# Optimization experiments

Hardware: AMD Instinct MI355X
Metric: run time of the kernel (lower is better)

## Reference

```python
import jax, jax.numpy as jnp
import numpy as np

D_MODEL = 1024
N_HEAD = 16
D_FF = 4096
SEG = 128  # hardcoded modality split length in the original module
EPS = 1e-5


def setup_inputs() -> dict:
    key = jax.random.key(0)
    ks = jax.random.split(key, 18)
    s = 0.02
    d, f = D_MODEL, D_FF
    inp = {
        "src": jax.random.normal(ks[0], (128, 256, d), dtype=jnp.float32),
        "Wq": jax.random.normal(ks[1], (d, d), dtype=jnp.float32) * s,
        "bq": jnp.zeros((d,), dtype=jnp.float32),
        "Wk": jax.random.normal(ks[2], (d, d), dtype=jnp.float32) * s,
        "bk": jnp.zeros((d,), dtype=jnp.float32),
        "Wv": jax.random.normal(ks[3], (d, d), dtype=jnp.float32) * s,
        "bv": jnp.zeros((d,), dtype=jnp.float32),
        "Wo": jax.random.normal(ks[4], (d, d), dtype=jnp.float32) * s,
        "bo": jnp.zeros((d,), dtype=jnp.float32),
        "W1": jax.random.normal(ks[5], (d, f), dtype=jnp.float32) * s,
        "b1": jnp.zeros((f,), dtype=jnp.float32),
        "W2": jax.random.normal(ks[6], (f, d), dtype=jnp.float32) * s,
        "b2": jnp.zeros((d,), dtype=jnp.float32),
        "g1": jnp.ones((SEG, d), dtype=jnp.float32),
        "beta1": jnp.zeros((SEG, d), dtype=jnp.float32),
        "g2": jnp.ones((SEG, d), dtype=jnp.float32),
        "beta2": jnp.zeros((SEG, d), dtype=jnp.float32),
    }
    return inp


def _mha(q_in, kv_in, Wq, bq, Wk, bk, Wv, bv, Wo, bo):
    B, Sq, d = q_in.shape
    Sk = kv_in.shape[1]
    dh = d // N_HEAD
    # project and split heads: [B, S, d] -> [B, H, S, dh]
    q = (q_in @ Wq + bq).reshape(B, Sq, N_HEAD, dh).transpose(0, 2, 1, 3)
    k = (kv_in @ Wk + bk).reshape(B, Sk, N_HEAD, dh).transpose(0, 2, 1, 3)
    v = (kv_in @ Wv + bv).reshape(B, Sk, N_HEAD, dh).transpose(0, 2, 1, 3)
    scores = jnp.einsum("bhqd,bhkd->bhqk", q, k) / jnp.sqrt(jnp.float32(dh))
    probs = jax.nn.softmax(scores, axis=-1)
    out = jnp.einsum("bhqk,bhkd->bhqd", probs, v)
    out = out.transpose(0, 2, 1, 3).reshape(B, Sq, d)
    return out @ Wo + bo


def _ln2d(x, g, b):
    # LayerNorm over last two dims (128, d_model), matching nn.LayerNorm((128, d))
    mu = jnp.mean(x, axis=(-2, -1), keepdims=True)
    var = jnp.mean(jnp.square(x - mu), axis=(-2, -1), keepdims=True)
    return (x - mu) * jax.lax.rsqrt(var + EPS) * g + b


def reference(src, Wq, bq, Wk, bk, Wv, bv, Wo, bo, W1, b1, W2, b2, g1, beta1, g2, beta2):
    modal1 = src[:, :SEG, :]
    modal2 = src[:, SEG:, :]

    def ffn(x):
        return jax.nn.relu(x @ W1 + b1) @ W2 + b2

    # modal1 attends to modal2
    m1 = modal1 + _mha(modal1, modal2, Wq, bq, Wk, bk, Wv, bv, Wo, bo)
    m1 = _ln2d(m1, g1, beta1)
    m1 = _ln2d(m1 + ffn(m1), g2, beta2)

    # modal2 attends to updated modal1
    m2 = modal2 + _mha(modal2, m1, Wq, bq, Wk, bk, Wv, bv, Wo, bo)
    m2 = _ln2d(m2, g1, beta1)
    m2 = _ln2d(m2 + ffn(m2), g2, beta2)

    return jnp.concatenate([m1, m2], axis=1)
```

## Files before the change

kernel.cpp:

```cpp
#include <hip/hip_runtime.h>
#include <stdint.h>

#define DEV __device__ __forceinline__

typedef __bf16 bf16x8 __attribute__((ext_vector_type(8)));
typedef float  f32x4  __attribute__((ext_vector_type(4)));

struct alignas(8) U16x4 { uint16_t x, y, z, w; };
struct alignas(16) U16x8 { uint16_t v[8]; };

DEV uint16_t f2bf(float f) {
  union { float f; uint32_t u; } v; v.f = f;
  uint32_t r = v.u + 0x7fffu + ((v.u >> 16) & 1u);
  return (uint16_t)(r >> 16);
}
DEV float bf2f(uint16_t u) {
  union { uint32_t u; float f; } v; v.u = ((uint32_t)u) << 16;
  return v.f;
}

DEV void gload16(const void* g, void* l) {
  __builtin_amdgcn_global_load_lds((__attribute__((address_space(1))) void*)(g),
                                   (__attribute__((address_space(3))) void*)(l),
                                   16, 0, 0);
}

__global__ __launch_bounds__(1024) void transpose_cvt(
    const float* __restrict__ in, uint16_t* __restrict__ out, int R, int C) {
  __shared__ float tile[32][33];
  const int tx = threadIdx.x, ty = threadIdx.y;
  const int r = blockIdx.y * 32 + ty, c = blockIdx.x * 32 + tx;
  tile[ty][tx] = in[(size_t)r * C + c];
  __syncthreads();
  const int oc = blockIdx.x * 32 + ty;
  const int orr = blockIdx.y * 32 + tx;
  out[(size_t)oc * R + orr] = f2bf(tile[tx][ty]);
}

__global__ __launch_bounds__(256) void cvt_modal(
    const float* __restrict__ src, uint16_t* __restrict__ m1, uint16_t* __restrict__ m2) {
  const int idx = blockIdx.x * 256 + threadIdx.x;
  const int E = idx * 4;
  const int t = E >> 10, dd = E & 1023;
  const size_t s1 = ((size_t)(t >> 7) * 256 + (t & 127)) * 1024 + dd;
  float4 a = *(const float4*)&src[s1];
  float4 b = *(const float4*)&src[s1 + 131072];
  U16x4 pa{f2bf(a.x), f2bf(a.y), f2bf(a.z), f2bf(a.w)};
  U16x4 pb{f2bf(b.x), f2bf(b.y), f2bf(b.z), f2bf(b.w)};
  *(U16x4*)&m1[E] = pa;
  *(U16x4*)&m2[E] = pb;
}

#define STA8(D, H, C, T) \
  gload16(Ac + (size_t)((H) * 2 + (C)) * kr64b + (size_t)(T) * 128 + aoff32, \
          &lds[(D) * 16384 + (H) * 8192 + (C) * 4096 + wS])
#define STB8(D, H, C, T) \
  gload16(Bc + (size_t)((H) * 2 + (C)) * kr64b + (size_t)(T) * 128 + boff32, \
          &lds[32768 + (D) * 16384 + (H) * 8192 + (C) * 4096 + wS])

#define PH8(Q, AB, BB, RDB, S1, S2, VMSTR)                                     \
  {                                                                            \
    if (RDB) {                                                                 \
      _Pragma("unroll") for (int n = 0; n < 4; ++n) {                          \
        bfr[n][0] = *(const bf16x8*)&lds[(BB) + bRow + n * 1024 + c0];         \
        bfr[n][1] = *(const bf16x8*)&lds[(BB) + bRow + n * 1024 + c1];         \
      }                                                                        \
    }                                                                          \
    _Pragma("unroll") for (int dm = 0; dm < 2; ++dm) {                         \
      afr[dm][0] = *(const bf16x8*)&lds[(AB) + aRow + ((Q) * 2 + dm) * 1024 + c0]; \
      afr[dm][1] = *(const bf16x8*)&lds[(AB) + aRow + ((Q) * 2 + dm) * 1024 + c1]; \
    }                                                                          \
    S1;                                                                        \
    S2;                                                                        \
    __builtin_amdgcn_s_barrier();                                              \
    asm volatile("s_waitcnt lgkmcnt(0)" ::: "memory");                         \
    __builtin_amdgcn_sched_barrier(0);                                         \
    __builtin_amdgcn_s_setprio(1);                                             \
    _Pragma("unroll") for (int dm = 0; dm < 2; ++dm)                           \
      _Pragma("unroll") for (int n = 0; n < 4; ++n) {                          \
        acc[(Q) * 2 + dm][n] = __builtin_amdgcn_mfma_f32_16x16x32_bf16(        \
            afr[dm][0], bfr[n][0], acc[(Q) * 2 + dm][n], 0, 0, 0);             \
        acc[(Q) * 2 + dm][n] = __builtin_amdgcn_mfma_f32_16x16x32_bf16(        \
            afr[dm][1], bfr[n][1], acc[(Q) * 2 + dm][n], 0, 0, 0);             \
      }                                                                        \
    __builtin_amdgcn_s_setprio(0);                                             \
    __builtin_amdgcn_sched_barrier(0);                                         \
    asm volatile(VMSTR ::: "memory");                                          \
    __builtin_amdgcn_s_barrier();                                              \
  }

#define ITER8(I, ST, VM4, VM8)                                                 \
  {                                                                            \
    const int t1 = 2 * (I) + 1, t2 = 2 * (I) + 2, t3 = 2 * (I) + 3;            \
    PH8(0, 0, 32768, 1, STA8(1, 0, 0, t1), STA8(1, 0, 1, t1), "")              \
    PH8(1, 0, 32768, 0, STA8(1, 1, 0, t1), STA8(1, 1, 1, t1), "")              \
    PH8(2, 0, 32768, 0, if (ST) STB8(0, 0, 0, t2), if (ST) STB8(0, 0, 1, t2), "") \
    PH8(3, 0, 32768, 0, if (ST) STB8(0, 1, 0, t2), if (ST) STB8(0, 1, 1, t2), VM4) \
    PH8(0, 16384, 49152, 1, if (ST) STA8(0, 0, 0, t2), if (ST) STA8(0, 0, 1, t2), "") \
    PH8(1, 16384, 49152, 0, if (ST) STA8(0, 1, 0, t2), if (ST) STA8(0, 1, 1, t2), "") \
    PH8(2, 16384, 49152, 0, if (ST) STB8(1, 0, 0, t3), if (ST) STB8(1, 0, 1, t3), "") \
    PH8(3, 16384, 49152, 0, if (ST) STB8(1, 1, 0, t3), if (ST) STB8(1, 1, 1, t3), VM8) \
  }

template <int RESID, bool RELU, bool OUTF32>
__global__ __launch_bounds__(512, 2) void gemm8p(
    const uint16_t* __restrict__ A, const uint16_t* __restrict__ Bt,
    const float* __restrict__ bias, const void* __restrict__ resid,
    void* __restrict__ outp, int N, int K, int nbn, int soff) {
  __shared__ __align__(16) uint16_t lds[65536];

  const int nwg = gridDim.x;
  const int s = (blockIdx.x & 7) * (nwg >> 3) + (blockIdx.x >> 3);
  const int bm = s / nbn, bn = s % nbn;
  const int brow = bm << 8, bcol = bn << 8;

  const int tid = threadIdx.x;
  const int w = tid >> 6, lane = tid & 63, l15 = lane & 15, lhi = lane >> 4;
  const int wm = w >> 2, wn = w & 3;

  const int cswz = (tid & 7) ^ ((tid >> 3) & 7);
  const uint32_t aoff32 =
      (uint32_t)(((size_t)(brow + (tid >> 3)) * (size_t)K + cswz * 8) * 2);
  const uint32_t boff32 =
      (uint32_t)(((size_t)(bcol + (tid >> 3)) * (size_t)K + cswz * 8) * 2);
  const char* Ac = (const char*)A;
  const char* Bc = (const char*)Bt;
  const uint32_t kr64b = (uint32_t)(64u * (uint32_t)K * 2u);
  const int wS = w * 512;

  const int c0 = (lhi ^ (l15 & 7)) * 8;
  const int c1 = c0 ^ 32;
  const int aRow = (wm * 128 + l15) * 64;
  const int bRow = (wn * 64 + l15) * 64;

  f32x4 acc[8][4];
  const f32x4 z = {0.f, 0.f, 0.f, 0.f};
#pragma unroll
  for (int m = 0; m < 8; ++m)
#pragma unroll
    for (int n = 0; n < 4; ++n) acc[m][n] = z;

  const int NI = K >> 7;

  STA8(0, 0, 0, 0); STA8(0, 0, 1, 0); STA8(0, 1, 0, 0); STA8(0, 1, 1, 0);
  STB8(0, 0, 0, 0); STB8(0, 0, 1, 0); STB8(0, 1, 0, 0); STB8(0, 1, 1, 0);
  STB8(1, 0, 0, 1); STB8(1, 0, 1, 1); STB8(1, 1, 0, 1); STB8(1, 1, 1, 1);
  asm volatile("s_waitcnt vmcnt(4)" ::: "memory");
  __builtin_amdgcn_s_barrier();
  __builtin_amdgcn_sched_barrier(0);

  {
    bf16x8 afr[2][2], bfr[4][2];
    int i = 0;
    for (; i < NI - 1; ++i)
      ITER8(i, true, "s_waitcnt vmcnt(4)", "s_waitcnt vmcnt(4)")
    ITER8(i, false, "s_waitcnt vmcnt(0)", "")
  }

#pragma unroll
  for (int n = 0; n < 4; ++n) {
    const int col = bcol + wn * 64 + n * 16 + l15;
    const float bs = bias[col];
#pragma unroll
    for (int m = 0; m < 8; ++m) {
#pragma unroll
      for (int r = 0; r < 4; ++r) {
        const int row = brow + wm * 128 + m * 16 + lhi * 4 + r;
        float v = acc[m][n][r] + bs;
        if (RELU) v = fmaxf(v, 0.f);
        if (RESID == 1) v += ((const float*)resid)[(size_t)row * 1024 + col];
        if (RESID == 2)
          v += ((const float*)resid)[((size_t)(row >> 7) * 256 + soff + (row & 127)) * 1024 + col];
        if (RESID == 3)
          v += bf2f(((const uint16_t*)resid)[(size_t)row * 1024 + col]);
        if (OUTF32)
          ((float*)outp)[(size_t)row * N + col] = v;
        else
          ((uint16_t*)outp)[(size_t)row * N + col] = f2bf(v);
      }
    }
  }
}

__global__ __launch_bounds__(256) void attn_kern(
    const uint16_t* __restrict__ Q, const uint16_t* __restrict__ KV,
    uint16_t* __restrict__ O) {
  __shared__ uint16_t sm[24576];
  uint16_t* sQ = sm;
  uint16_t* sK = sm + 8192;
  uint16_t* sVt = sm + 16384;
  uint16_t* sP = sm;
  const int bh = blockIdx.x, b = bh >> 4, h = bh & 15;
  const int tid = threadIdx.x, w = tid >> 6, lane = tid & 63, l15 = lane & 15, lhi = lane >> 4;
  const size_t base = (size_t)b * 131072 + h * 64;
  const size_t bkv = (size_t)b * 262144 + h * 64;

  for (int i = 0; i < 4; ++i) {
    const int gidx = i * 256 + tid;
    const int row = gidx >> 3, co = (gidx & 7) * 8;
    *(uint4*)&sQ[row * 64 + co] = *(const uint4*)&Q[base + (size_t)row * 1024 + co];
    *(uint4*)&sK[row * 64 + co] = *(const uint4*)&KV[bkv + (size_t)row * 2048 + co];
  }
  {
    const int r = tid >> 1, cb = (tid & 1) * 32;
    for (int jj = 0; jj < 4; ++jj) {
      uint4 vv = *(const uint4*)&KV[bkv + 1024 + (size_t)r * 2048 + cb + jj * 8];
      const uint16_t* e = (const uint16_t*)&vv;
      for (int j = 0; j < 8; ++j) sVt[(cb + jj * 8 + j) * 128 + r] = e[j];
    }
  }
  __syncthreads();

  f32x4 s[2][8];
  const f32x4 z = {0.f, 0.f, 0.f, 0.f};
  for (int m = 0; m < 2; ++m)
    for (int n = 0; n < 8; ++n) s[m][n] = z;
#pragma unroll
  for (int kk = 0; kk < 2; ++kk) {
    bf16x8 aq[2];
#pragma unroll
    for (int m = 0; m < 2; ++m)
      aq[m] = *(const bf16x8*)&sQ[(w * 32 + m * 16 + l15) * 64 + kk * 32 + lhi * 8];
#pragma unroll
    for (int n = 0; n < 8; ++n) {
      bf16x8 bk = *(const bf16x8*)&sK[(n * 16 + l15) * 64 + kk * 32 + lhi * 8];
#pragma unroll
      for (int m = 0; m < 2; ++m)
        s[m][n] = __builtin_amdgcn_mfma_f32_16x16x32_bf16(aq[m], bk, s[m][n], 0, 0, 0);
    }
  }

  for (int m = 0; m < 2; ++m) {
    float mx[4], sum[4];
#pragma unroll
    for (int r = 0; r < 4; ++r) {
      float v = s[m][0][r];
      for (int n = 1; n < 8; ++n) v = fmaxf(v, s[m][n][r]);
      for (int msk = 1; msk < 16; msk <<= 1) v = fmaxf(v, __shfl_xor(v, msk, 64));
      mx[r] = v;
      sum[r] = 0.f;
    }
    for (int n = 0; n < 8; ++n)
      for (int r = 0; r < 4; ++r) {
        float e = __expf((s[m][n][r] - mx[r]) * 0.125f);
        s[m][n][r] = e;
        sum[r] += e;
      }
#pragma unroll
    for (int r = 0; r < 4; ++r) {
      float t = sum[r];
      for (int msk = 1; msk < 16; msk <<= 1) t += __shfl_xor(t, msk, 64);
      sum[r] = 1.f / t;
    }
    for (int n = 0; n < 8; ++n)
      for (int r = 0; r < 4; ++r) s[m][n][r] *= sum[r];
  }
  __syncthreads();

  for (int m = 0; m < 2; ++m)
    for (int n = 0; n < 8; ++n)
      for (int r = 0; r < 4; ++r)
        sP[(w * 32 + m * 16 + lhi * 4 + r) * 128 + n * 16 + l15] = f2bf(s[m][n][r]);
  __syncthreads();

  f32x4 o[2][4];
  for (int m = 0; m < 2; ++m)
    for (int n = 0; n < 4; ++n) o[m][n] = z;
#pragma unroll
  for (int kk = 0; kk < 4; ++kk) {
    bf16x8 ap[2];
#pragma unroll
    for (int m = 0; m < 2; ++m)
      ap[m] = *(const bf16x8*)&sP[(w * 32 + m * 16 + l15) * 128 + kk * 32 + lhi * 8];
#pragma unroll
    for (int n = 0; n < 4; ++n) {
      bf16x8 bv = *(const bf16x8*)&sVt[(n * 16 + l15) * 128 + kk * 32 + lhi * 8];
#pragma unroll
      for (int m = 0; m < 2; ++m)
        o[m][n] = __builtin_amdgcn_mfma_f32_16x16x32_bf16(ap[m], bv, o[m][n], 0, 0, 0);
    }
  }
  for (int m = 0; m < 2; ++m)
    for (int n = 0; n < 4; ++n)
      for (int r = 0; r < 4; ++r) {
        const int q = w * 32 + m * 16 + lhi * 4 + r, c = n * 16 + l15;
        O[base + (size_t)q * 1024 + c] = f2bf(o[m][n][r]);
      }
}

__global__ __launch_bounds__(256) void ln_stats(
    const uint16_t* __restrict__ x, float* __restrict__ pstats) {
  const int b = blockIdx.x >> 2, q = blockIdx.x & 3, tid = threadIdx.x;
  const uint16_t* xb = x + (size_t)b * 131072 + q * 32768;
  float s = 0.f, ss = 0.f;
  for (int i = tid; i < 4096; i += 256) {
    U16x8 v = *(const U16x8*)&xb[i * 8];
#pragma unroll
    for (int j = 0; j < 8; ++j) {
      float f = bf2f(v.v[j]);
      s += f;
      ss += f * f;
    }
  }
#pragma unroll
  for (int m = 1; m < 64; m <<= 1) {
    s += __shfl_xor(s, m, 64);
    ss += __shfl_xor(ss, m, 64);
  }
  __shared__ float red[8];
  const int w = tid >> 6;
  if ((tid & 63) == 0) { red[w] = s; red[4 + w] = ss; }
  __syncthreads();
  if (tid == 0) {
    pstats[blockIdx.x * 2] = red[0] + red[1] + red[2] + red[3];
    pstats[blockIdx.x * 2 + 1] = red[4] + red[5] + red[6] + red[7];
  }
}

template <bool FINAL>
__global__ __launch_bounds__(256) void ln_apply(
    const uint16_t* __restrict__ x, const float* __restrict__ g,
    const float* __restrict__ bet, const float* __restrict__ pstats,
    uint16_t* __restrict__ outbf, float* __restrict__ outf) {
  const int b = blockIdx.x >> 4, c = blockIdx.x & 15, tid = threadIdx.x;
  float S = 0.f, SS = 0.f;
#pragma unroll
  for (int k = 0; k < 4; ++k) {
    S += pstats[b * 8 + k * 2];
    SS += pstats[b * 8 + k * 2 + 1];
  }
  const float mu = S * (1.f / 131072.f);
  const float rs = rsqrtf(SS * (1.f / 131072.f) - mu * mu + 1e-5f);
  const size_t xb = (size_t)b * 131072;
#pragma unroll
  for (int j = 0; j < 4; ++j) {
    const int o = c * 8192 + (j * 256 + tid) * 8;
    U16x8 v = *(const U16x8*)&x[xb + o];
    float4 g0 = *(const float4*)&g[o], g1 = *(const float4*)&g[o + 4];
    float4 b0 = *(const float4*)&bet[o], b1 = *(const float4*)&bet[o + 4];
    float r[8];
    r[0] = (bf2f(v.v[0]) - mu) * rs * g0.x + b0.x;
    r[1] = (bf2f(v.v[1]) - mu) * rs * g0.y + b0.y;
    r[2] = (bf2f(v.v[2]) - mu) * rs * g0.z + b0.z;
    r[3] = (bf2f(v.v[3]) - mu) * rs * g0.w + b0.w;
    r[4] = (bf2f(v.v[4]) - mu) * rs * g1.x + b1.x;
    r[5] = (bf2f(v.v[5]) - mu) * rs * g1.y + b1.y;
    r[6] = (bf2f(v.v[6]) - mu) * rs * g1.z + b1.z;
    r[7] = (bf2f(v.v[7]) - mu) * rs * g1.w + b1.w;
    if (FINAL) {
      float4 o0{r[0], r[1], r[2], r[3]}, o1{r[4], r[5], r[6], r[7]};
      float* of = outf + (size_t)b * 262144 + o;
      *(float4*)&of[0] = o0;
      *(float4*)&of[4] = o1;
      if (outbf) {
        U16x8 u;
#pragma unroll
        for (int i = 0; i < 8; ++i) u.v[i] = f2bf(r[i]);
        *(U16x8*)&outbf[xb + o] = u;
      }
    } else {
      U16x8 u;
#pragma unroll
      for (int i = 0; i < 8; ++i) u.v[i] = f2bf(r[i]);
      *(U16x8*)&outbf[xb + o] = u;
    }
  }
}

extern "C" void kernel_launch(void* const* d_in, const int* in_sizes, int n_in,
                              void* d_out, int out_size, void* d_ws, size_t ws_size,
                              hipStream_t stream) {
  const float* src = (const float*)d_in[0];
  const float* Wq = (const float*)d_in[1];
  const float* bq = (const float*)d_in[2];
  const float* Wk = (const float*)d_in[3];
  const float* bk = (const float*)d_in[4];
  const float* Wv = (const float*)d_in[5];
  const float* bv = (const float*)d_in[6];
  const float* Wo = (const float*)d_in[7];
  const float* bo = (const float*)d_in[8];
  const float* W1 = (const float*)d_in[9];
  const float* b1 = (const float*)d_in[10];
  const float* W2 = (const float*)d_in[11];
  const float* b2 = (const float*)d_in[12];
  const float* g1 = (const float*)d_in[13];
  const float* be1 = (const float*)d_in[14];
  const float* g2 = (const float*)d_in[15];
  const float* be2 = (const float*)d_in[16];
  float* dout = (float*)d_out;
  char* ws = (char*)d_ws;

  const size_t MB = 1024 * 1024;
  uint16_t* wq_t = (uint16_t*)(ws + 0 * MB);
  uint16_t* wkv_t = (uint16_t*)(ws + 2 * MB);
  uint16_t* wv_t = (uint16_t*)(ws + 4 * MB);
  uint16_t* wo_t = (uint16_t*)(ws + 6 * MB);
  uint16_t* w1_t = (uint16_t*)(ws + 8 * MB);
  uint16_t* w2_t = (uint16_t*)(ws + 16 * MB);
  uint16_t* m1bf = (uint16_t*)(ws + 24 * MB);
  uint16_t* mod2 = (uint16_t*)(ws + 56 * MB);
  uint16_t* QB = (uint16_t*)(ws + 88 * MB);
  uint16_t* KVB = (uint16_t*)(ws + 120 * MB);
  uint16_t* ATT = (uint16_t*)(ws + 184 * MB);
  float* bkvp = (float*)(ws + 184 * MB);
  uint16_t* Hbf = QB;
  uint16_t* mod1 = (uint16_t*)(ws + 216 * MB);
  uint16_t* XAb = (uint16_t*)(ws + 248 * MB);
  uint16_t* YBF = (uint16_t*)(ws + 280 * MB);
  float* pstats = (float*)(ws + 312 * MB);

  dim3 tb(32, 32);
  transpose_cvt<<<dim3(32, 32), tb, 0, stream>>>(Wq, wq_t, 1024, 1024);
  transpose_cvt<<<dim3(32, 32), tb, 0, stream>>>(Wk, wkv_t, 1024, 1024);
  transpose_cvt<<<dim3(32, 32), tb, 0, stream>>>(Wv, wv_t, 1024, 1024);
  transpose_cvt<<<dim3(32, 32), tb, 0, stream>>>(Wo, wo_t, 1024, 1024);
  transpose_cvt<<<dim3(128, 32), tb, 0, stream>>>(W1, w1_t, 1024, 4096);
  transpose_cvt<<<dim3(32, 128), tb, 0, stream>>>(W2, w2_t, 4096, 1024);
  cvt_modal<<<16384, 256, 0, stream>>>(src, mod1, mod2);

  auto phase = [&](const uint16_t* qsrc, const uint16_t* kvsrc, int soff,
                   float* out_f, uint16_t* out_bf) {
    gemm8p<0, false, false><<<256, 512, 0, stream>>>(qsrc, wq_t, bq, nullptr, QB,
                                                     1024, 1024, 4, 0);
    hipMemcpyAsync(bkvp, bk, 4096, hipMemcpyDeviceToDevice, stream);
    hipMemcpyAsync(bkvp + 1024, bv, 4096, hipMemcpyDeviceToDevice, stream);
    gemm8p<0, false, false><<<512, 512, 0, stream>>>(kvsrc, wkv_t, bkvp, nullptr, KVB,
                                                     2048, 1024, 8, 0);
    attn_kern<<<2048, 256, 0, stream>>>(QB, KVB, ATT);
    gemm8p<2, false, false><<<256, 512, 0, stream>>>(ATT, wo_t, bo, src, XAb,
                                                     1024, 1024, 4, soff);
    ln_stats<<<512, 256, 0, stream>>>(XAb, pstats);
    ln_apply<false><<<2048, 256, 0, stream>>>(XAb, g1, be1, pstats, YBF, nullptr);
    gemm8p<0, true, false><<<1024, 512, 0, stream>>>(YBF, w1_t, b1, nullptr, Hbf,
                                                     4096, 1024, 16, 0);
    gemm8p<3, false, false><<<256, 512, 0, stream>>>(Hbf, w2_t, b2, YBF, XAb,
                                                     1024, 4096, 4, 0);
    ln_stats<<<512, 256, 0, stream>>>(XAb, pstats);
    ln_apply<true><<<2048, 256, 0, stream>>>(XAb, g2, be2, pstats, out_bf, out_f);
  };

  phase(mod1, mod2, 0, dout, m1bf);
  phase(mod2, m1bf, 128, dout + 131072, nullptr);

  (void)in_sizes; (void)n_in; (void)out_size; (void)ws_size;
}
```

Baseline: 1.204 ms.

## Add 1024-thread 256x256 GEMM with 4-stage LDS pipeline for FFN

Introduces a new gemm256 kernel using 16 waves per block, 256x256 output tiles, a 4-deep K-slice ring buffer in LDS loaded via global_load_lds, swizzled LDS layout, and setprio around MFMA bursts. The two FFN GEMMs now use it instead of gemm8p. The aim is more data reuse per block and better overlap of global loads with MFMA. It uses one barrier per K-step with 32-wide K tiles and a direct, uncoalesced epilogue store, which may limit gains.

New measurement: 1.218 ms. Within noise of the previous version (+1.1%).

```diff
diff --git a/kernel.cpp b/kernel.cpp
--- a/kernel.cpp
+++ b/kernel.cpp
@@ -49,6 +49,112 @@
   U16x4 pb{f2bf(b.x), f2bf(b.y), f2bf(b.z), f2bf(b.w)};
   *(U16x4*)&m1[E] = pa;
   *(U16x4*)&m2[E] = pb;
+}
+
+#define TILE2(T, ST, WAITSTR)                                                   \
+  {                                                                             \
+    const int abase = ((T) & 3) * 8192;                                         \
+    const int bbase = 32768 + ((T) & 3) * 8192;                                 \
+    bf16x8 afr[4], bfr[4];                                                      \
+    _Pragma("unroll") for (int n = 0; n < 4; ++n)                               \
+        bfr[n] = *(const bf16x8*)&lds[bbase + boff + n * 512];                  \
+    _Pragma("unroll") for (int m = 0; m < 4; ++m)                               \
+        afr[m] = *(const bf16x8*)&lds[abase + aoff + m * 512];                  \
+    asm volatile(WAITSTR ::: "memory");                                         \
+    __builtin_amdgcn_s_barrier();                                               \
+    if (ST) {                                                                   \
+      const int kn = ((T) + 3) << 5;                                            \
+      const int sb = (((T) + 3) & 3) * 8192;                                    \
+      gload16(gA + kn, &lds[sb + wS]);                                          \
+      gload16(gB + kn, &lds[32768 + sb + wS]);                                  \
+    }                                                                           \
+    asm volatile("s_waitcnt lgkmcnt(0)" ::: "memory");                          \
+    __builtin_amdgcn_sched_barrier(0);                                          \
+    __builtin_amdgcn_s_setprio(1);                                              \
+    _Pragma("unroll") for (int m = 0; m < 4; ++m)                               \
+        _Pragma("unroll") for (int n = 0; n < 4; ++n)                           \
+        acc[m][n] = __builtin_amdgcn_mfma_f32_16x16x32_bf16(afr[m], bfr[n],     \
+                                                            acc[m][n], 0, 0, 0);\
+    __builtin_amdgcn_s_setprio(0);                                              \
+    __builtin_amdgcn_sched_barrier(0);                                          \
+  }
+
+template <int RESID, bool RELU, bool OUTF32>
+__global__ __launch_bounds__(1024, 1) void gemm256(
+    const uint16_t* __restrict__ A, const uint16_t* __restrict__ Bt,
+    const float* __restrict__ bias, const void* __restrict__ resid,
+    void* __restrict__ outp, int N, int K, int nbn, int soff) {
+  __shared__ __align__(16) uint16_t lds[65536];
+
+  const int nwg = gridDim.x;
+  const int s = (blockIdx.x & 7) * (nwg >> 3) + (blockIdx.x >> 3);
+  const int bm = s / nbn, bn = s % nbn;
+  const int brow = bm << 8, bcol = bn << 8;
+
+  const int tid = threadIdx.x;
+  const int w = tid >> 6, lane = tid & 63, l15 = lane & 15, lhi = lane >> 4;
+  const int wm = w >> 2, wn = w & 3;
+
+  const int srow = tid >> 2;
+  const int cswz = (tid & 3) ^ ((tid >> 3) & 3);
+  const uint16_t* gA = A + (size_t)(brow + srow) * K + cswz * 8;
+  const uint16_t* gB = Bt + (size_t)(bcol + srow) * K + cswz * 8;
+  const int wS = w * 512;
+
+  const int p = lhi ^ ((l15 >> 1) & 3);
+  const int aoff = (wm * 64 + l15) * 32 + p * 8;
+  const int boff = (wn * 64 + l15) * 32 + p * 8;
+
+  f32x4 acc[4][4];
+  const f32x4 z = {0.f, 0.f, 0.f, 0.f};
+#pragma unroll
+  for (int m = 0; m < 4; ++m)
+#pragma unroll
+    for (int n = 0; n < 4; ++n) acc[m][n] = z;
+
+  const int nt = K >> 5;
+
+#pragma unroll
+  for (int pt = 0; pt < 3; ++pt) {
+    const int sb = pt * 8192, kk = pt << 5;
+    gload16(gA + kk, &lds[sb + wS]);
+    gload16(gB + kk, &lds[32768 + sb + wS]);
+  }
+  asm volatile("s_waitcnt vmcnt(4)" ::: "memory");
+  __builtin_amdgcn_s_barrier();
+  __builtin_amdgcn_sched_barrier(0);
+
+  int t = 0;
+  for (; t < nt - 3; ++t) TILE2(t, true, "s_waitcnt vmcnt(2)");
+  TILE2(t, false, "s_waitcnt vmcnt(2)");
+  ++t;
+  TILE2(t, false, "s_waitcnt vmcnt(0)");
+  ++t;
+  TILE2(t, false, "");
+
+#pragma unroll
+  for (int n = 0; n < 4; ++n) {
+    const int col = bcol + wn * 64 + n * 16 + l15;
+    const float bs = bias[col];
+#pragma unroll
+    for (int m = 0; m < 4; ++m) {
+#pragma unroll
+      for (int r = 0; r < 4; ++r) {
+        const int row = brow + wm * 64 + m * 16 + lhi * 4 + r;
+        float v = acc[m][n][r] + bs;
+        if (RELU) v = fmaxf(v, 0.f);
+        if (RESID == 1) v += ((const float*)resid)[(size_t)row * 1024 + col];
+        if (RESID == 2)
+          v += ((const float*)resid)[((size_t)(row >> 7) * 256 + soff + (row & 127)) * 1024 + col];
+        if (RESID == 3)
+          v += bf2f(((const uint16_t*)resid)[(size_t)row * 1024 + col]);
+        if (OUTF32)
+          ((float*)outp)[(size_t)row * N + col] = v;
+        else
+          ((uint16_t*)outp)[(size_t)row * N + col] = f2bf(v);
+      }
+    }
+  }
 }
 
 #define STA8(D, H, C, T) \
@@ -431,10 +537,10 @@
                                                      1024, 1024, 4, soff);
     ln_stats<<<512, 256, 0, stream>>>(XAb, pstats);
     ln_apply<false><<<2048, 256, 0, stream>>>(XAb, g1, be1, pstats, YBF, nullptr);
-    gemm8p<0, true, false><<<1024, 512, 0, stream>>>(YBF, w1_t, b1, nullptr, Hbf,
-                                                     4096, 1024, 16, 0);
-    gemm8p<3, false, false><<<256, 512, 0, stream>>>(Hbf, w2_t, b2, YBF, XAb,
-                                                     1024, 4096, 4, 0);
+    gemm256<0, true, false><<<1024, 1024, 0, stream>>>(YBF, w1_t, b1, nullptr, Hbf,
+                                                       4096, 1024, 16, 0);
+    gemm256<3, false, false><<<256, 1024, 0, stream>>>(Hbf, w2_t, b2, YBF, XAb,
+                                                       1024, 4096, 4, 0);
     ln_stats<<<512, 256, 0, stream>>>(XAb, pstats);
     ln_apply<true><<<2048, 256, 0, stream>>>(XAb, g2, be2, pstats, out_bf, out_f);
   };
```
